# Performance work log

Measured on AMD Instinct MI355X. Metric: run time of the kernel, lower is better.

## Reference

```python
import jax, jax.numpy as jnp
import numpy as np

N, E, ESM, H, OUT, L, NG = 20000, 640000, 1280, 128, 256, 3, 64
NV, EV = 4, 1  # node/edge vector channels
MSG_S, MSG_V = 2 * H + H, 2 * NV + EV   # 384, 9
UPD_S, UPD_V = 2 * H, 2 * NV            # 256, 8


def _safe_norm(v):
    # exact ||v|| with zero (not nan) gradient at v == 0
    n2 = jnp.sum(v * v, axis=-1)
    pos = n2 > 0
    return jnp.sqrt(jnp.where(pos, n2, 1.0)) * pos


def _normalize(x, eps=1e-12):
    n = _safe_norm(x)[..., None]
    return jnp.where(n > 0, x / jnp.maximum(n, eps), 0.0)


def _ln(x, g, b, eps=1e-5):
    m = x.mean(-1, keepdims=True)
    v = ((x - m) ** 2).mean(-1, keepdims=True)
    return (x - m) / jnp.sqrt(v + eps) * g + b


def _gvp(s, v, Wss, Wvs, Wsv, Wvv, g, b):
    # s: [M, Cs], v: [M, Cv, 3]
    vn = _safe_norm(v)                                        # [M, Cv]
    s_out = jax.nn.gelu(_ln(s @ Wss.T + vn @ Wvs.T, g, b), approximate=False)
    v_out = jnp.einsum('mic,oi->moc', v, Wvv)                 # [M, Cvo, 3]
    v_out = v_out * jax.nn.sigmoid(s @ Wsv.T)[:, :, None]     # gate from input s
    return s_out, v_out


def _compute_node_vectors(coords, cb):
    ca_cb = _normalize(cb - coords)
    ca_next = jnp.roll(coords, -1, axis=0)
    d = (ca_next - coords).at[-1].set(0.0)
    d = _normalize(d)
    normal = _normalize(jnp.cross(ca_cb, d))
    t = (ca_next - jnp.roll(coords, 1, axis=0)).at[0].set(0.0).at[-1].set(0.0)
    t = _normalize(t)
    return jnp.stack([ca_cb, d, normal, t], axis=1)           # [N, 4, 3]


def setup_inputs() -> dict:
    key = jax.random.key(0)
    ks = jax.random.split(key, 32)

    def w(k, shape):
        return (jax.random.normal(k, shape, jnp.float32) / np.sqrt(shape[-1])).astype(jnp.float32)

    inp = {
        'esm_features': jax.random.normal(ks[0], (N, ESM), jnp.float32),
        'geometric_features': jax.random.normal(ks[1], (N, 15), jnp.float32),
        'node_coords': jax.random.normal(ks[2], (N, 3), jnp.float32) * 10.0,
        'edge_index': jax.random.randint(ks[3], (2, E), 0, N, jnp.int32),
        'edge_attr': jax.random.normal(ks[4], (E, 16), jnp.float32),
        'batch_index': jnp.sort(jax.random.randint(ks[5], (N,), 0, NG, jnp.int32)),
        # projections
        'node_proj_W': w(ks[6], (H, ESM + 9)), 'node_proj_b': jnp.zeros((H,), jnp.float32),
        'edge_proj_W': w(ks[7], (H, 13)), 'edge_proj_b': jnp.zeros((H,), jnp.float32),
        # message GVP (stacked over L layers)
        'msg_Wss': w(ks[8], (L, H, MSG_S)), 'msg_Wvs': w(ks[9], (L, H, MSG_V)),
        'msg_Wsv': w(ks[10], (L, NV, MSG_S)), 'msg_Wvv': w(ks[11], (L, NV, MSG_V)),
        'msg_ln_g': jnp.ones((L, H), jnp.float32), 'msg_ln_b': jnp.zeros((L, H), jnp.float32),
        # update GVP
        'upd_Wss': w(ks[12], (L, H, UPD_S)), 'upd_Wvs': w(ks[13], (L, H, UPD_V)),
        'upd_Wsv': w(ks[14], (L, NV, UPD_S)), 'upd_Wvv': w(ks[15], (L, NV, UPD_V)),
        'upd_ln_g': jnp.ones((L, H), jnp.float32), 'upd_ln_b': jnp.zeros((L, H), jnp.float32),
        # heads
        'node_out_W': w(ks[16], (ESM, H)), 'node_out_b': jnp.zeros((ESM,), jnp.float32),
        'graph_out_W': w(ks[17], (OUT, H)), 'graph_out_b': jnp.zeros((OUT,), jnp.float32),
    }
    return inp


def reference(esm_features, geometric_features, node_coords, edge_index, edge_attr,
              batch_index, node_proj_W, node_proj_b, edge_proj_W, edge_proj_b,
              msg_Wss, msg_Wvs, msg_Wsv, msg_Wvv, msg_ln_g, msg_ln_b,
              upd_Wss, upd_Wvs, upd_Wsv, upd_Wvv, upd_ln_g, upd_ln_b,
              node_out_W, node_out_b, graph_out_W, graph_out_b):
    n = esm_features.shape[0]
    cb = geometric_features[:, 3:6]
    geo_scalar = geometric_features[:, 6:15]
    node_s = jnp.concatenate([esm_features, geo_scalar], -1) @ node_proj_W.T + node_proj_b
    node_v = _compute_node_vectors(node_coords, cb)
    edge_s = jnp.concatenate([edge_attr[:, 0:2], edge_attr[:, 5:]], -1) @ edge_proj_W.T + edge_proj_b
    edge_v = edge_attr[:, 2:5][:, None, :]                    # [E, 1, 3]
    src, dst = edge_index[0], edge_index[1]
    for l in range(msg_Wss.shape[0]):
        ms = jnp.concatenate([node_s[src], node_s[dst], edge_s], -1)   # [E, 3H]
        mv = jnp.concatenate([node_v[src], node_v[dst], edge_v], 1)    # [E, 9, 3]
        ms, mv = _gvp(ms, mv, msg_Wss[l], msg_Wvs[l], msg_Wsv[l], msg_Wvv[l],
                      msg_ln_g[l], msg_ln_b[l])
        ag_s = jnp.zeros((n, ms.shape[1]), ms.dtype).at[dst].add(ms)
        ag_v = jnp.zeros((n, mv.shape[1], 3), mv.dtype).at[dst].add(mv)
        us = jnp.concatenate([node_s, ag_s], -1)
        uv = jnp.concatenate([node_v, ag_v], 1)
        ns, nv = _gvp(us, uv, upd_Wss[l], upd_Wvs[l], upd_Wsv[l], upd_Wvv[l],
                      upd_ln_g[l], upd_ln_b[l])
        node_s = node_s + ns
        node_v = node_v + nv
    updated_nodes = node_s @ node_out_W.T + node_out_b
    gfeat = node_s @ graph_out_W.T + graph_out_b
    cnt = jax.ops.segment_sum(jnp.ones((n,), gfeat.dtype), batch_index, NG)
    graph_emb = jax.ops.segment_sum(gfeat, batch_index, NG) / jnp.maximum(cnt, 1.0)[:, None]
    return graph_emb, updated_nodes
```

## Files before the change

### kernel.cpp

```cpp
#include <hip/hip_runtime.h>
#include <math.h>

#define DEVI __device__ __forceinline__

namespace {

constexpr int NN = 20000;
constexpr int NE = 640000;

typedef __attribute__((ext_vector_type(8))) short s8v;
typedef __attribute__((ext_vector_type(4))) float f4v;

DEVI float gelu_f(float x){ return 0.5f*x*(1.0f+erff(x*0.70710678118654752440f)); }
DEVI float gelu_t(float x){
  float u = x*x;
  float z = x*(1.59576912f + 0.07135481f*u);
  return x / (1.f + __expf(-z));
}
DEVI float sigm(float x){ return 1.0f/(1.0f+expf(-x)); }
DEVI float sigm_f(float x){ return 1.0f/(1.0f+__expf(-x)); }
DEVI unsigned bf_rne(float f){ unsigned u=__float_as_uint(f); return (u + 0x7fffu + ((u>>16)&1u)) >> 16; }

struct F3{ float x,y,z; };
DEVI F3 sub3(F3 a, F3 b){ return F3{a.x-b.x, a.y-b.y, a.z-b.z}; }
DEVI F3 cross3(F3 a, F3 b){ return F3{a.y*b.z-a.z*b.y, a.z*b.x-a.x*b.z, a.x*b.y-a.y*b.x}; }
DEVI F3 snorm3(F3 v){
  float n2 = v.x*v.x+v.y*v.y+v.z*v.z;
  if(n2 > 0.f){ float inv = 1.0f/sqrtf(n2); return F3{v.x*inv, v.y*inv, v.z*inv}; }
  return F3{0.f,0.f,0.f};
}

__global__ void k_prep(const float* __restrict__ npW, const float* __restrict__ noW,
                       const float* __restrict__ goW,
                       const float* __restrict__ mWss, const float* __restrict__ mWvs,
                       const float* __restrict__ uWss, const float* __restrict__ uWvs,
                       unsigned short* __restrict__ npW_bf, float* __restrict__ Wt_no,
                       float* __restrict__ Wt_go,
                       float* __restrict__ Wt_mss, float* __restrict__ Wt_mvs,
                       float* __restrict__ Wt_uss, float* __restrict__ Wt_uvs){
  int b = blockIdx.x, t = threadIdx.x;
  if(b >= 1563){
    int idx = (b-1563)*256 + t;
    if(idx < 128*1289) npW_bf[idx] = (unsigned short)bf_rne(npW[idx]);
    return;
  }
  const float* src; float* dst; int R,C,ld,base,elems;
  if(b<640){ src=noW; dst=Wt_no; R=1280;C=128;ld=128; base=0; elems=163840; }
  else if(b<768){ src=goW; dst=Wt_go; R=256;C=128;ld=128; base=640; elems=32768; }
  else {
    int bb=b-768; int l=bb/265; int r=bb-l*265;
    if(r<128){ src=mWss+(size_t)l*128*384; dst=Wt_mss+(size_t)l*256*128; R=128;C=256;ld=384; base=768+l*265; elems=32768; }
    else if(r<133){ src=mWvs+(size_t)l*128*9; dst=Wt_mvs+(size_t)l*9*128; R=128;C=9;ld=9; base=768+l*265+128; elems=1152; }
    else if(r<261){ src=uWss+(size_t)l*128*256; dst=Wt_uss+(size_t)l*256*128; R=128;C=256;ld=256; base=768+l*265+133; elems=32768; }
    else { src=uWvs+(size_t)l*128*8; dst=Wt_uvs+(size_t)l*8*128; R=128;C=8;ld=8; base=768+l*265+261; elems=1024; }
  }
  int idx=(b-base)*256+t;
  if(idx>=elems) return;
  int r=idx/C, c=idx%C;
  dst[c*R+r] = src[r*ld+c];
}

__global__ __launch_bounds__(256,2) void k_init(
    const float* __restrict__ esm, const float* __restrict__ geo,
    const unsigned short* __restrict__ npW_bf, const float* __restrict__ bias,
    float* __restrict__ node_s){
  __shared__ unsigned short A_lds[64][136];
  __shared__ unsigned short B_lds[128][136];
  int t = threadIdx.x;
  int n0 = blockIdx.x*64;
  int wv = t>>6, lane = t&63;
  int kpair = t&63;
  int rb = t>>6;
  f4v acc[8];
#pragma unroll
  for(int i=0;i<8;i++) acc[i] = (f4v){0.f,0.f,0.f,0.f};
  for(int k0=0; k0<1408; k0+=128){
#pragma unroll
    for(int i=0;i<16;i++){
      int r = rb + 4*i;
      int row = n0 + r;
      int kk = k0 + 2*kpair;
      float v0=0.f, v1=0.f;
      if(row < NN){
        if(kk < 1280)        v0 = esm[(size_t)row*1280+kk];
        else if(kk < 1289)   v0 = geo[row*15+6+(kk-1280)];
        if(kk+1 < 1280)      v1 = esm[(size_t)row*1280+kk+1];
        else if(kk+1 < 1289) v1 = geo[row*15+6+(kk+1-1280)];
      }
      *reinterpret_cast<unsigned*>(&A_lds[r][2*kpair]) = bf_rne(v0) | (bf_rne(v1)<<16);
    }
#pragma unroll
    for(int i=0;i<32;i++){
      int o = rb + 4*i;
      int kk = k0 + 2*kpair;
      unsigned w0 = (kk<1289)   ? (unsigned)npW_bf[(size_t)o*1289+kk]   : 0u;
      unsigned w1 = (kk+1<1289) ? (unsigned)npW_bf[(size_t)o*1289+kk+1] : 0u;
      *reinterpret_cast<unsigned*>(&B_lds[o][2*kpair]) = w0 | (w1<<16);
    }
    __syncthreads();
    int arow = wv*16 + (lane&15);
    int kb = (lane>>4)*8;
#pragma unroll
    for(int s=0;s<4;s++){
      s8v a = *reinterpret_cast<const s8v*>(&A_lds[arow][s*32+kb]);
#pragma unroll
      for(int nt=0;nt<8;nt++){
        s8v b = *reinterpret_cast<const s8v*>(&B_lds[nt*16+(lane&15)][s*32+kb]);
        acc[nt] = __builtin_amdgcn_mfma_f32_16x16x32_bf16(a, b, acc[nt], 0,0,0);
      }
    }
    __syncthreads();
  }
  int col = lane&15;
  int r4 = (lane>>4)*4;
#pragma unroll
  for(int nt=0;nt<8;nt++){
    int o = nt*16+col;
    float bsv = bias[o];
#pragma unroll
    for(int r=0;r<4;r++){
      int row = n0 + wv*16 + r4 + r;
      if(row<NN) node_s[(size_t)row*128+o] = acc[nt][r] + bsv;
    }
  }
}

__global__ void k_nodevec(const float* __restrict__ coords, const float* __restrict__ geo,
                          float* __restrict__ node_v,
                          int* __restrict__ counts, int* __restrict__ cntg){
  int n = blockIdx.x*256 + threadIdx.x;
  if(n<64) cntg[n]=0;
  if(n>=NN) return;
  counts[n]=0;
  F3 c  {coords[n*3], coords[n*3+1], coords[n*3+2]};
  F3 cb {geo[n*15+3], geo[n*15+4], geo[n*15+5]};
  F3 cacb = snorm3(sub3(cb, c));
  F3 d{0.f,0.f,0.f};
  if(n < NN-1){
    F3 nx {coords[(n+1)*3], coords[(n+1)*3+1], coords[(n+1)*3+2]};
    d = snorm3(sub3(nx, c));
  }
  F3 nor = snorm3(cross3(cacb, d));
  F3 tv{0.f,0.f,0.f};
  if(n>0 && n<NN-1){
    F3 nx {coords[(n+1)*3], coords[(n+1)*3+1], coords[(n+1)*3+2]};
    F3 pv {coords[(n-1)*3], coords[(n-1)*3+1], coords[(n-1)*3+2]};
    tv = snorm3(sub3(nx, pv));
  }
  float* p = node_v + n*12;
  p[0]=cacb.x; p[1]=cacb.y; p[2]=cacb.z;
  p[3]=d.x;    p[4]=d.y;    p[5]=d.z;
  p[6]=nor.x;  p[7]=nor.y;  p[8]=nor.z;
  p[9]=tv.x;   p[10]=tv.y;  p[11]=tv.z;
}

__global__ void k_hist(const int* __restrict__ eidx, const int* __restrict__ batch,
                       int* __restrict__ counts, int* __restrict__ cntg){
  int i = blockIdx.x*256+threadIdx.x;
  if(i<NE) atomicAdd(&counts[eidx[NE+i]], 1);
  if(i<NN) atomicAdd(&cntg[batch[i]], 1);
}
__global__ void k_scan1(const int* __restrict__ counts, int* __restrict__ bsums){
  __shared__ int red[256];
  int b=blockIdx.x, t=threadIdx.x;
  int base=b*512;
  int v=0;
  for(int i=t;i<512;i+=256){ int g=base+i; if(g<NN) v+=counts[g]; }
  red[t]=v; __syncthreads();
  for(int s=128;s;s>>=1){ if(t<s) red[t]+=red[t+s]; __syncthreads(); }
  if(t==0) bsums[b]=red[0];
}
__global__ void k_scan23(const int* __restrict__ counts, const int* __restrict__ bsums,
                         int* __restrict__ offs, int* __restrict__ cursor){
  __shared__ int c_l[512];
  int b=blockIdx.x, t=threadIdx.x, base=b*512;
  for(int i=t;i<512;i+=256){ int g=base+i; c_l[i] = (g<NN)? counts[g]:0; }
  __syncthreads();
  if(t==0){
    int run=0;
    for(int i=0;i<b;i++) run += bsums[i];
    for(int i=0;i<512;i++){
      int g=base+i;
      if(g<NN){ offs[g]=run; cursor[g]=run; }
      run += c_l[i];
    }
    if(b==39) offs[NN]=run;
  }
}
__global__ void k_fill(const int* __restrict__ eidx, int* __restrict__ cursor,
                       const float* __restrict__ eattr,
                       int* __restrict__ srcp, float* __restrict__ ea_s){
  int e = blockIdx.x*256+threadIdx.x;
  if(e>=NE) return;
  int d = eidx[NE+e];
  int s = eidx[e];
  int pos = atomicAdd(&cursor[d], 1);
  srcp[pos] = s;
  const float4* src4 = reinterpret_cast<const float4*>(eattr + (size_t)e*16);
  float4* dst4 = reinterpret_cast<float4*>(ea_s + (size_t)pos*16);
  dst4[0]=src4[0]; dst4[1]=src4[1]; dst4[2]=src4[2]; dst4[3]=src4[3];
}

__global__ __launch_bounds__(256,4) void k_pre(
                      const float* __restrict__ node_s, const float* __restrict__ node_v,
                      const float* __restrict__ Wt_ss, const float* __restrict__ Wt_vs,
                      const float* __restrict__ Wsv, const float* __restrict__ Wvv,
                      float* __restrict__ P_a, float* __restrict__ P_b,
                      float* __restrict__ G_a, float* __restrict__ G_b,
                      float* __restrict__ V_a, float* __restrict__ V_b){
  __shared__ float s_l[16][128];
  __shared__ float nv_l[16][4];
  __shared__ float uv[16][12];
  int t = threadIdx.x;
  int n0 = blockIdx.x*16;
  for(int idx=t; idx<2048; idx+=256){
    int n = idx>>7, k = idx&127;
    s_l[n][k] = node_s[(size_t)(n0+n)*128 + k];
  }
  if(t<192){ int n=t/12, k=t%12; uv[n][k] = node_v[(n0+n)*12+k]; }
  __syncthreads();
  if(t<64){
    int n=t>>2, j=t&3;
    float x=uv[n][j*3], y=uv[n][j*3+1], z=uv[n][j*3+2];
    float n2=x*x+y*y+z*z;
    nv_l[n][j] = n2>0.f ? sqrtf(n2) : 0.f;
  }
  if(t<192){
    int n=t/12, k=t%12, c=k/3, x=k-c*3;
    float va=0.f, vb=0.f;
#pragma unroll
    for(int j=0;j<4;j++){
      float vv = uv[n][j*3+x];
      va += Wvv[c*9+j]*vv;
      vb += Wvv[c*9+4+j]*vv;
    }
    V_a[(n0+n)*12+k]=va; V_b[(n0+n)*12+k]=vb;
  }
  if(t<128){
    int n=t>>3, c=(t>>1)&3, hh=t&1;
    const float* w = Wsv + c*384 + hh*128;
    float g=0.f;
    for(int k=0;k<128;k+=4){
      float4 s4 = *reinterpret_cast<const float4*>(&s_l[n][k]);
      g = fmaf(s4.x,w[k],g); g = fmaf(s4.y,w[k+1],g);
      g = fmaf(s4.z,w[k+2],g); g = fmaf(s4.w,w[k+3],g);
    }
    (hh ? G_b : G_a)[(n0+n)*4+c] = g;
  }
  __syncthreads();
  int o = t&127, h = t>>7;
  float acc[16];
#pragma unroll
  for(int i=0;i<16;i++) acc[i]=0.f;
  const float* Wb = Wt_ss + h*128*128;
  for(int k=0;k<128;k+=4){
    float w0=Wb[(k+0)*128+o], w1=Wb[(k+1)*128+o], w2=Wb[(k+2)*128+o], w3=Wb[(k+3)*128+o];
#pragma unroll
    for(int n=0;n<16;n++){
      float4 s4 = *reinterpret_cast<const float4*>(&s_l[n][k]);
      acc[n] = fmaf(s4.x,w0,acc[n]); acc[n] = fmaf(s4.y,w1,acc[n]);
      acc[n] = fmaf(s4.z,w2,acc[n]); acc[n] = fmaf(s4.w,w3,acc[n]);
    }
  }
  const float* Wv = Wt_vs + h*4*128;
#pragma unroll
  for(int j=0;j<4;j++){
    float w = Wv[j*128+o];
#pragma unroll
    for(int n=0;n<16;n++) acc[n] += nv_l[n][j]*w;
  }
  float* P = h ? P_b : P_a;
#pragma unroll
  for(int n=0;n<16;n++) P[(size_t)(n0+n)*128+o] = acc[n];
}

__global__ void k_econst3(const float* __restrict__ mWss, const float* __restrict__ mWvs,
                          const float* __restrict__ mWsv, const float* __restrict__ mWvv,
                          const float* __restrict__ Wep, const float* __restrict__ epb,
                          float* __restrict__ econ){
  int l = blockIdx.x;
  const float* Wss = mWss + (size_t)l*128*384;
  const float* Wvs = mWvs + (size_t)l*128*9;
  const float* Wsv = mWsv + (size_t)l*4*384;
  const float* Wvv = mWvv + (size_t)l*4*9;
  float* ec = econ + (size_t)l*2048;
  int t=threadIdx.x;
  for(int idx=t; idx<13*128; idx+=256){
    int j=idx>>7, o=idx&127;
    float s=0.f;
    for(int k=0;k<128;k++) s += Wss[o*384+256+k]*Wep[k*13+j];
    ec[j*128+o]=s;
  }
  for(int o=t;o<128;o+=256){
    float s=0.f;
    for(int k=0;k<128;k++) s += Wss[o*384+256+k]*epb[k];
    ec[1664+o]=s;
    ec[1792+o]=Wvs[o*9+8];
  }
  if(t<52){ int c=t/13,j=t%13; float s=0.f; for(int k=0;k<128;k++) s+=Wsv[c*384+256+k]*Wep[k*13+j]; ec[1920+t]=s; }
  if(t<4){ float s=0.f; for(int k=0;k<128;k++) s+=Wsv[t*384+256+k]*epb[k]; ec[1972+t]=s; ec[1976+t]=Wvv[t*9+8]; }
}

__global__ __launch_bounds__(256,4) void k_edge(
    const float* __restrict__ ea_s, const float* __restrict__ ec,
    unsigned* __restrict__ preS2, float* __restrict__ preG){
  int t = threadIdx.x;
  int lane = t&63;
  int wid = blockIdx.x*4 + (t>>6);
  float mex[13], mey[13];
#pragma unroll
  for(int j=0;j<13;j++){ mex[j]=ec[j*128+lane]; mey[j]=ec[j*128+64+lane]; }
  float bx=ec[1664+lane], by=ec[1664+64+lane];
  float w8x=ec[1792+lane], w8y=ec[1792+64+lane];
  int cg = (lane<4)?lane:0;
  float grc[13];
#pragma unroll
  for(int j=0;j<13;j++) grc[j]=ec[1920+cg*13+j];
  float gb = ec[1972+cg];
  int e00 = wid*8;
#pragma unroll 2
  for(int i=0;i<8;i++){
    int e = e00+i;
    const float4* ea = reinterpret_cast<const float4*>(ea_s + (size_t)e*16);
    float4 A0=ea[0], A1=ea[1], A2=ea[2], A3=ea[3];
    float e0=A0.x,e1=A0.y,e2=A1.y,e3=A1.z,e4=A1.w,
          e5=A2.x,e6=A2.y,e7=A2.z,e8=A2.w,e9=A3.x,
          e10=A3.y,e11=A3.z,e12=A3.w;
    float evx=A0.z, evy=A0.w, evz=A1.x;
    float en2 = evx*evx+evy*evy+evz*evz;
    float evn = en2>0.f ? sqrtf(en2) : 0.f;
    float px = fmaf(evn,w8x,bx);
    float py = fmaf(evn,w8y,by);
    px=fmaf(mex[0],e0,px);   py=fmaf(mey[0],e0,py);
    px=fmaf(mex[1],e1,px);   py=fmaf(mey[1],e1,py);
    px=fmaf(mex[2],e2,px);   py=fmaf(mey[2],e2,py);
    px=fmaf(mex[3],e3,px);   py=fmaf(mey[3],e3,py);
    px=fmaf(mex[4],e4,px);   py=fmaf(mey[4],e4,py);
    px=fmaf(mex[5],e5,px);   py=fmaf(mey[5],e5,py);
    px=fmaf(mex[6],e6,px);   py=fmaf(mey[6],e6,py);
    px=fmaf(mex[7],e7,px);   py=fmaf(mey[7],e7,py);
    px=fmaf(mex[8],e8,px);   py=fmaf(mey[8],e8,py);
    px=fmaf(mex[9],e9,px);   py=fmaf(mey[9],e9,py);
    px=fmaf(mex[10],e10,px); py=fmaf(mey[10],e10,py);
    px=fmaf(mex[11],e11,px); py=fmaf(mey[11],e11,py);
    px=fmaf(mex[12],e12,px); py=fmaf(mey[12],e12,py);
    preS2[(size_t)e*64+lane] = bf_rne(px) | (bf_rne(py)<<16);
    if(lane<4){
      float g=gb;
      g=fmaf(grc[0],e0,g);  g=fmaf(grc[1],e1,g);  g=fmaf(grc[2],e2,g);
      g=fmaf(grc[3],e3,g);  g=fmaf(grc[4],e4,g);  g=fmaf(grc[5],e5,g);
      g=fmaf(grc[6],e6,g);  g=fmaf(grc[7],e7,g);  g=fmaf(grc[8],e8,g);
      g=fmaf(grc[9],e9,g);  g=fmaf(grc[10],e10,g); g=fmaf(grc[11],e11,g);
      g=fmaf(grc[12],e12,g);
      preG[(size_t)e*8+lane] = g;
    } else if(lane<7){
      float evv = (lane==4)?evx:((lane==5)?evy:evz);
      preG[(size_t)e*8+lane] = evv;
    }
  }
}

#define DECLST(P) unsigned P##w=0; float P##pax=0.f,P##pay=0.f,P##g8=0.f,P##ev=0.f,P##ga=0.f,P##va=0.f;
#define LOADST(P, IDX) do{ int _p=(IDX); int _s=srcp[_p]; \
  P##w   = preS2[(size_t)_p*64 + lane]; \
  P##pax = P_a[(size_t)_s*128+lane]; P##pay = P_a[(size_t)_s*128+64+lane]; \
  if(lane<12){ P##g8 = preG[(size_t)_p*8+cv]; P##ev = preG[(size_t)_p*8+4+xv]; \
               P##ga = G_a[(size_t)_s*4+cv];  P##va = V_a[(size_t)_s*12+lane]; } \
}while(0)
#define COMPUTE(P) do{ \
  float px = __uint_as_float(P##w<<16); \
  float py = __uint_as_float(P##w & 0xffff0000u); \
  float pre0 = px + P##pax + PBx; \
  float pre1 = py + P##pay + PBy; \
  float sm = pre0+pre1; \
  float sq = pre0*pre0 + pre1*pre1; \
  _Pragma("unroll") \
  for(int m=32;m;m>>=1){ sm += __shfl_xor(sm,m); sq += __shfl_xor(sq,m); } \
  float mean = sm*0.0078125f; \
  float var  = fmaf(sq,0.0078125f, -mean*mean); \
  float rstd = rsqrtf((var>0.f?var:0.f) + 1e-5f); \
  accx += gelu_t(fmaf((pre0-mean)*rstd, LGx, LBx)); \
  accy += gelu_t(fmaf((pre1-mean)*rstd, LGy, LBy)); \
  if(lane<12){ \
    float g = P##g8 + P##ga + gbn; \
    float gt = sigm_f(g); \
    avk = fmaf(fmaf(wvc, P##ev, P##va + vbk), gt, avk); \
  } \
}while(0)

__global__ __launch_bounds__(256,4) void k_msg(
                      const float* __restrict__ P_a, const float* __restrict__ P_b,
                      const float* __restrict__ G_a, const float* __restrict__ G_b,
                      const float* __restrict__ V_a, const float* __restrict__ V_b,
                      const unsigned* __restrict__ preS2, const float* __restrict__ preG,
                      const int* __restrict__ srcp, const int* __restrict__ offs,
                      const float* __restrict__ ec,
                      const float* __restrict__ lng, const float* __restrict__ lnb,
                      float* __restrict__ ag_s, float* __restrict__ ag_v){
  int t = threadIdx.x;
  int n = blockIdx.x*4 + (t>>6);
  int lane = t&63;
  float PBx = P_b[(size_t)n*128+lane], PBy = P_b[(size_t)n*128+64+lane];
  float LGx = lng[lane], LGy = lng[64+lane];
  float LBx = lnb[lane], LBy = lnb[64+lane];
  int cv = lane/3, xv = lane - cv*3;
  float vbk=0.f, gbn=0.f, wvc=0.f;
  if(lane<12){
    vbk = V_b[(size_t)n*12+lane];
    gbn = G_b[(size_t)n*4+cv];
    wvc = ec[1976+cv];
  }
  float accx=0.f, accy=0.f, avk=0.f;
  int beg = offs[n], end = offs[n+1];
  DECLST(a_) DECLST(b_)
  int idx = beg;
  if(beg < end) LOADST(a_, beg);
  while(idx + 1 < end){
    LOADST(b_, idx+1);
    COMPUTE(a_);
    if(idx + 2 < end) LOADST(a_, idx+2);
    COMPUTE(b_);
    idx += 2;
  }
  if(idx < end) COMPUTE(a_);
  ag_s[(size_t)n*128+lane]    = accx;
  ag_s[(size_t)n*128+64+lane] = accy;
  if(lane<12) ag_v[(size_t)n*12+lane] = avk;
}

__global__ __launch_bounds__(256,4) void k_update(
                         float* __restrict__ node_s, float* __restrict__ node_v,
                         const float* __restrict__ ag_s, const float* __restrict__ ag_v,
                         const float* __restrict__ Wt_ss, const float* __restrict__ Wt_vs,
                         const float* __restrict__ Wsv, const float* __restrict__ Wvv,
                         const float* __restrict__ lng, const float* __restrict__ lnb){
  __shared__ float us[16][260];
  __shared__ float pre[16][129];
  __shared__ float uv[16][24];
  __shared__ float uvn[16][8];
  __shared__ float stats[16][2];
  __shared__ float gate_l[16][4];
  int t = threadIdx.x;
  int n0 = blockIdx.x*16;
  for(int idx=t; idx<2048; idx+=256){
    int n = idx>>7, k = idx&127;
    us[n][k]     = node_s[(size_t)(n0+n)*128+k];
    us[n][128+k] = ag_s[(size_t)(n0+n)*128+k];
  }
  for(int idx=t; idx<384; idx+=256){
    int n = idx/24, k = idx%24;
    uv[n][k] = (k<12) ? node_v[(n0+n)*12+k] : ag_v[(n0+n)*12 + (k-12)];
  }
  __syncthreads();
  if(t<128){
    int n=t>>3, j=t&7;
    float x=uv[n][j*3], y=uv[n][j*3+1], z=uv[n][j*3+2];
    float n2=x*x+y*y+z*z;
    uvn[n][j] = n2>0.f ? sqrtf(n2) : 0.f;
  }
  __syncthreads();
  int o = t&127, h = t>>7;
  float acc[8];
#pragma unroll
  for(int i=0;i<8;i++) acc[i]=0.f;
  for(int k=0;k<256;k+=4){
    float w0=Wt_ss[(k+0)*128+o], w1=Wt_ss[(k+1)*128+o], w2=Wt_ss[(k+2)*128+o], w3=Wt_ss[(k+3)*128+o];
#pragma unroll
    for(int i=0;i<8;i++){
      float4 s4 = *reinterpret_cast<const float4*>(&us[h*8+i][k]);
      acc[i] = fmaf(s4.x,w0,acc[i]); acc[i] = fmaf(s4.y,w1,acc[i]);
      acc[i] = fmaf(s4.z,w2,acc[i]); acc[i] = fmaf(s4.w,w3,acc[i]);
    }
  }
#pragma unroll
  for(int j=0;j<8;j++){
    float w = Wt_vs[j*128+o];
#pragma unroll
    for(int i=0;i<8;i++) acc[i] += uvn[h*8+i][j]*w;
  }
#pragma unroll
  for(int i=0;i<8;i++) pre[h*8+i][o] = acc[i];
  __syncthreads();
  {
    int n = t>>4, p = t&15;
    float s=0.f;
#pragma unroll
    for(int q=0;q<8;q++) s += pre[n][p*8+q];
#pragma unroll
    for(int m=8;m;m>>=1) s += __shfl_xor(s,m);
    float mean = s*(1.f/128.f);
    float v=0.f;
#pragma unroll
    for(int q=0;q<8;q++){ float d=pre[n][p*8+q]-mean; v += d*d; }
#pragma unroll
    for(int m=8;m;m>>=1) v += __shfl_xor(v,m);
    if(p==0){ stats[n][0]=mean; stats[n][1]=rsqrtf(v*(1.f/128.f)+1e-5f); }
  }
  __syncthreads();
  {
    float LG = lng[o], LB = lnb[o];
#pragma unroll
    for(int i=0;i<8;i++){
      int n = h*8+i;
      float hh = (pre[n][o]-stats[n][0])*stats[n][1]*LG + LB;
      node_s[(size_t)(n0+n)*128+o] += gelu_f(hh);
    }
  }
  {
    int n = t>>4, c = t&3, p = (t>>2)&3;
    float g=0.f;
    int kb = p*64;
    for(int k=0;k<64;k+=4){
      float4 s4 = *reinterpret_cast<const float4*>(&us[n][kb+k]);
      g = fmaf(s4.x,Wsv[c*256+kb+k],g);   g = fmaf(s4.y,Wsv[c*256+kb+k+1],g);
      g = fmaf(s4.z,Wsv[c*256+kb+k+2],g); g = fmaf(s4.w,Wsv[c*256+kb+k+3],g);
    }
    g += __shfl_xor(g,4);
    g += __shfl_xor(g,8);
    if(p==0) gate_l[n][c] = sigm(g);
  }
  __syncthreads();
  if(t<192){
    int n = t/12, k = t%12, c = k/3, x = k-c*3;
    float s=0.f;
#pragma unroll
    for(int j=0;j<8;j++) s += Wvv[c*8+j]*uv[n][j*3+x];
    node_v[(n0+n)*12+k] += s*gate_l[n][c];
  }
}

__global__ __launch_bounds__(256,4) void k_outg(
                      const float* __restrict__ node_s, const float* __restrict__ Wt_no,
                      const float* __restrict__ nob, const float* __restrict__ Wt_go,
                      const int* __restrict__ batch, float* __restrict__ gacc,
                      float* __restrict__ out){
  __shared__ float s_l[16][128];
  __shared__ int b_l[16];
  int t = threadIdx.x;
  int n0 = blockIdx.x*16;
  int y = blockIdx.y;
  for(int idx=t; idx<2048; idx+=256){
    int n=idx>>7, k=idx&127;
    s_l[n][k] = node_s[(size_t)(n0+n)*128+k];
  }
  if(y==5 && t<16) b_l[t]=batch[n0+t];
  __syncthreads();
  if(y<5){
    int o = y*256 + t;
    float acc[16];
#pragma unroll
    for(int i=0;i<16;i++) acc[i]=0.f;
    for(int k=0;k<128;k+=4){
      float w0=Wt_no[(k+0)*1280+o], w1=Wt_no[(k+1)*1280+o], w2=Wt_no[(k+2)*1280+o], w3=Wt_no[(k+3)*1280+o];
#pragma unroll
      for(int n=0;n<16;n++){
        float4 s4 = *reinterpret_cast<const float4*>(&s_l[n][k]);
        acc[n] = fmaf(s4.x,w0,acc[n]); acc[n] = fmaf(s4.y,w1,acc[n]);
        acc[n] = fmaf(s4.z,w2,acc[n]); acc[n] = fmaf(s4.w,w3,acc[n]);
      }
    }
    float b = nob[o];
#pragma unroll
    for(int n=0;n<16;n++) out[16384 + (size_t)(n0+n)*1280 + o] = acc[n]+b;
  } else {
    int o=t;
    float acc[16];
#pragma unroll
    for(int i=0;i<16;i++) acc[i]=0.f;
    for(int k=0;k<128;k+=4){
      float w0=Wt_go[(k+0)*256+o], w1=Wt_go[(k+1)*256+o], w2=Wt_go[(k+2)*256+o], w3=Wt_go[(k+3)*256+o];
#pragma unroll
      for(int n=0;n<16;n++){
        float4 s4 = *reinterpret_cast<const float4*>(&s_l[n][k]);
        acc[n] = fmaf(s4.x,w0,acc[n]); acc[n] = fmaf(s4.y,w1,acc[n]);
        acc[n] = fmaf(s4.z,w2,acc[n]); acc[n] = fmaf(s4.w,w3,acc[n]);
      }
    }
    float run=0.f; int cur=b_l[0];
#pragma unroll
    for(int n=0;n<16;n++){
      int g=b_l[n];
      if(g!=cur){ atomicAdd(&gacc[cur*256+o], run); run=0.f; cur=g; }
      run += acc[n];
    }
    atomicAdd(&gacc[cur*256+o], run);
  }
}

__global__ void k_gfin(const float* __restrict__ gacc, const int* __restrict__ cntg,
                       const float* __restrict__ gob, float* __restrict__ out){
  int g=blockIdx.x, o=threadIdx.x;
  int c=cntg[g];
  out[g*256+o] = (c>0) ? (gacc[g*256+o]/(float)c + gob[o]) : 0.f;
}

}

extern "C" void kernel_launch(void* const* d_in, const int* in_sizes, int n_in,
                              void* d_out, int out_size, void* d_ws, size_t ws_size,
                              hipStream_t stream){
  (void)in_sizes; (void)n_in; (void)out_size;
  const float* esm   = (const float*)d_in[0];
  const float* geo   = (const float*)d_in[1];
  const float* coords= (const float*)d_in[2];
  const int*   eidx  = (const int*)d_in[3];
  const float* eattr = (const float*)d_in[4];
  const int*   batch = (const int*)d_in[5];
  const float* npW   = (const float*)d_in[6];
  const float* npb   = (const float*)d_in[7];
  const float* epW   = (const float*)d_in[8];
  const float* epb   = (const float*)d_in[9];
  const float* mWss  = (const float*)d_in[10];
  const float* mWvs  = (const float*)d_in[11];
  const float* mWsv  = (const float*)d_in[12];
  const float* mWvv  = (const float*)d_in[13];
  const float* mlg   = (const float*)d_in[14];
  const float* mlb   = (const float*)d_in[15];
  const float* uWss  = (const float*)d_in[16];
  const float* uWvs  = (const float*)d_in[17];
  const float* uWsv  = (const float*)d_in[18];
  const float* uWvv  = (const float*)d_in[19];
  const float* ulg   = (const float*)d_in[20];
  const float* ulb   = (const float*)d_in[21];
  const float* noW   = (const float*)d_in[22];
  const float* nob   = (const float*)d_in[23];
  const float* goW   = (const float*)d_in[24];
  const float* gob   = (const float*)d_in[25];
  float* out = (float*)d_out;

  char* base = (char*)d_ws;
  size_t off = 0;
  auto ALLOC = [&](size_t bytes)->char*{
    char* p = base + off;
    off = (off + bytes + 255) & ~(size_t)255;
    return p;
  };
  float* node_s = (float*)ALLOC((size_t)NN*128*4);
  float* P_a    = (float*)ALLOC((size_t)NN*128*4);
  float* P_b    = (float*)ALLOC((size_t)NN*128*4);
  float* ag_s   = (float*)ALLOC((size_t)NN*128*4);
  float* node_v = (float*)ALLOC((size_t)NN*12*4);
  float* ag_v   = (float*)ALLOC((size_t)NN*12*4);
  float* V_a    = (float*)ALLOC((size_t)NN*12*4);
  float* V_b    = (float*)ALLOC((size_t)NN*12*4);
  float* G_a    = (float*)ALLOC((size_t)NN*4*4);
  float* G_b    = (float*)ALLOC((size_t)NN*4*4);
  unsigned short* npW_bf = (unsigned short*)ALLOC((size_t)128*1289*2);
  float* Wt_no  = (float*)ALLOC((size_t)128*1280*4);
  float* Wt_go  = (float*)ALLOC((size_t)128*256*4);
  float* Wt_mss = (float*)ALLOC((size_t)3*256*128*4);
  float* Wt_mvs = (float*)ALLOC((size_t)3*9*128*4);
  float* Wt_uss = (float*)ALLOC((size_t)3*256*128*4);
  float* Wt_uvs = (float*)ALLOC((size_t)3*8*128*4);
  float* econ   = (float*)ALLOC((size_t)3*2048*4);
  float* gacc   = (float*)ALLOC((size_t)64*256*4);
  int* counts = (int*)ALLOC((size_t)NN*4);
  int* offs   = (int*)ALLOC((size_t)(NN+1)*4);
  int* cursor = (int*)ALLOC((size_t)NN*4);
  int* bsums  = (int*)ALLOC((size_t)64*4);
  int* cntg   = (int*)ALLOC((size_t)64*4);
  int* srcp   = (int*)ALLOC((size_t)NE*4);
  float* ea_s = (float*)ALLOC((size_t)NE*16*4);
  unsigned* preS2 = (unsigned*)ALLOC((size_t)NE*64*4);
  float* preG     = (float*)ALLOC((size_t)NE*8*4);
  if(off > ws_size) return;

  hipMemsetAsync(gacc, 0, (size_t)64*256*4, stream);

  k_prep<<<2208,256,0,stream>>>(npW, noW, goW, mWss, mWvs, uWss, uWvs,
                                npW_bf, Wt_no, Wt_go, Wt_mss, Wt_mvs, Wt_uss, Wt_uvs);
  k_init<<<313,256,0,stream>>>(esm, geo, npW_bf, npb, node_s);
  k_nodevec<<<79,256,0,stream>>>(coords, geo, node_v, counts, cntg);
  k_hist<<<2500,256,0,stream>>>(eidx, batch, counts, cntg);
  k_scan1<<<40,256,0,stream>>>(counts, bsums);
  k_scan23<<<40,256,0,stream>>>(counts, bsums, offs, cursor);
  k_fill<<<2500,256,0,stream>>>(eidx, cursor, eattr, srcp, ea_s);
  k_econst3<<<3,256,0,stream>>>(mWss, mWvs, mWsv, mWvv, epW, epb, econ);

  for(int l=0;l<3;l++){
    k_pre<<<1250,256,0,stream>>>(node_s, node_v,
                                 Wt_mss + (size_t)l*256*128, Wt_mvs + (size_t)l*9*128,
                                 mWsv + (size_t)l*4*384, mWvv + (size_t)l*4*9,
                                 P_a, P_b, G_a, G_b, V_a, V_b);
    k_edge<<<20000,256,0,stream>>>(ea_s, econ + (size_t)l*2048, preS2, preG);
    k_msg<<<5000,256,0,stream>>>(P_a, P_b, G_a, G_b, V_a, V_b, preS2, preG, srcp, offs,
                                 econ + (size_t)l*2048, mlg + (size_t)l*128, mlb + (size_t)l*128,
                                 ag_s, ag_v);
    k_update<<<1250,256,0,stream>>>(node_s, node_v, ag_s, ag_v,
                                    Wt_uss + (size_t)l*256*128, Wt_uvs + (size_t)l*8*128,
                                    uWsv + (size_t)l*4*256, uWvv + (size_t)l*4*8,
                                    ulg + (size_t)l*128, ulb + (size_t)l*128);
  }
  k_outg<<<dim3(1250,6),256,0,stream>>>(node_s, Wt_no, nob, Wt_go, batch, gacc, out);
  k_gfin<<<64,256,0,stream>>>(gacc, cntg, gob, out);
}
```

Measured before the change: 1.705 ms.

## Pre-convert ESM to bf16 and split-K the input projection GEMM

Adds a separate conversion kernel that writes the ESM and geometric features as a padded bf16 matrix, and pads the projection weights to the same K. The input projection GEMM now reads operands straight from global memory with vectorized loads, without LDS staging or barriers, and splits K four ways to raise the block count. A new reduce kernel sums the four partials, adds the bias, and writes node_s, reusing the preS2 buffer as scratch. This is meant to remove the serialized, poorly coalesced load-and-convert path in the old GEMM, at the cost of an extra bf16 copy of the inputs and partial-sum traffic through memory.

Result: faster. 1.627 ms (-4.6%).

```diff
diff --git a/kernel.cpp b/kernel.cpp
--- a/kernel.cpp
+++ b/kernel.cpp
@@ -41,7 +41,10 @@
   int b = blockIdx.x, t = threadIdx.x;
   if(b >= 1563){
     int idx = (b-1563)*256 + t;
-    if(idx < 128*1289) npW_bf[idx] = (unsigned short)bf_rne(npW[idx]);
+    if(idx < 128*1408){
+      int r = idx/1408, c = idx-r*1408;
+      npW_bf[idx] = (c<1289) ? (unsigned short)bf_rne(npW[(size_t)r*1289+c]) : (unsigned short)0;
+    }
     return;
   }
   const float* src; float* dst; int R,C,ld,base,elems;
@@ -60,69 +63,77 @@
   dst[c*R+r] = src[r*ld+c];
 }
 
-__global__ __launch_bounds__(256,2) void k_init(
-    const float* __restrict__ esm, const float* __restrict__ geo,
-    const unsigned short* __restrict__ npW_bf, const float* __restrict__ bias,
-    float* __restrict__ node_s){
-  __shared__ unsigned short A_lds[64][136];
-  __shared__ unsigned short B_lds[128][136];
+__global__ void k_conv(const float* __restrict__ esm, const float* __restrict__ geo,
+                       unsigned short* __restrict__ esm_bf){
+  int idx = blockIdx.x*256 + threadIdx.x;
+  if(idx >= 20000*176) return;
+  int r = idx/176, c = idx - r*176;
+  int k = c*8;
+  float v0,v1,v2,v3,v4,v5,v6,v7;
+  if(k+8 <= 1280){
+    const float4* p = reinterpret_cast<const float4*>(esm + (size_t)r*1280 + k);
+    float4 x=p[0], y=p[1];
+    v0=x.x;v1=x.y;v2=x.z;v3=x.w;v4=y.x;v5=y.y;v6=y.z;v7=y.w;
+  } else {
+    float vv[8];
+#pragma unroll
+    for(int j=0;j<8;j++){
+      int kk=k+j;
+      vv[j] = (kk<1280)? esm[(size_t)r*1280+kk] : ((kk<1289)? geo[r*15+6+(kk-1280)] : 0.f);
+    }
+    v0=vv[0];v1=vv[1];v2=vv[2];v3=vv[3];v4=vv[4];v5=vv[5];v6=vv[6];v7=vv[7];
+  }
+  uint4 w;
+  w.x = bf_rne(v0) | (bf_rne(v1)<<16);
+  w.y = bf_rne(v2) | (bf_rne(v3)<<16);
+  w.z = bf_rne(v4) | (bf_rne(v5)<<16);
+  w.w = bf_rne(v6) | (bf_rne(v7)<<16);
+  reinterpret_cast<uint4*>(esm_bf)[idx] = w;
+}
+
+__global__ __launch_bounds__(256,4) void k_init(
+    const unsigned short* __restrict__ esm_bf, const unsigned short* __restrict__ npW_bf,
+    float* __restrict__ part){
   int t = threadIdx.x;
-  int n0 = blockIdx.x*64;
+  int b = blockIdx.x;
+  int ks = b & 3, nb = b >> 2;
   int wv = t>>6, lane = t&63;
-  int kpair = t&63;
-  int rb = t>>6;
+  int row0 = nb*64 + wv*16;
+  int arow = row0 + (lane&15);
+  int arc = (arow < NN) ? arow : (NN-1);
+  int kb = (lane>>4)*8;
+  const unsigned short* ap = esm_bf + (size_t)arc*1408 + ks*352 + kb;
+  const unsigned short* bp = npW_bf + (size_t)(lane&15)*1408 + ks*352 + kb;
   f4v acc[8];
 #pragma unroll
   for(int i=0;i<8;i++) acc[i] = (f4v){0.f,0.f,0.f,0.f};
-  for(int k0=0; k0<1408; k0+=128){
-#pragma unroll
-    for(int i=0;i<16;i++){
-      int r = rb + 4*i;
-      int row = n0 + r;
-      int kk = k0 + 2*kpair;
-      float v0=0.f, v1=0.f;
-      if(row < NN){
-        if(kk < 1280)        v0 = esm[(size_t)row*1280+kk];
-        else if(kk < 1289)   v0 = geo[row*15+6+(kk-1280)];
-        if(kk+1 < 1280)      v1 = esm[(size_t)row*1280+kk+1];
-        else if(kk+1 < 1289) v1 = geo[row*15+6+(kk+1-1280)];
-      }
-      *reinterpret_cast<unsigned*>(&A_lds[r][2*kpair]) = bf_rne(v0) | (bf_rne(v1)<<16);
-    }
-#pragma unroll
-    for(int i=0;i<32;i++){
-      int o = rb + 4*i;
-      int kk = k0 + 2*kpair;
-      unsigned w0 = (kk<1289)   ? (unsigned)npW_bf[(size_t)o*1289+kk]   : 0u;
-      unsigned w1 = (kk+1<1289) ? (unsigned)npW_bf[(size_t)o*1289+kk+1] : 0u;
-      *reinterpret_cast<unsigned*>(&B_lds[o][2*kpair]) = w0 | (w1<<16);
-    }
-    __syncthreads();
-    int arow = wv*16 + (lane&15);
-    int kb = (lane>>4)*8;
-#pragma unroll
-    for(int s=0;s<4;s++){
-      s8v a = *reinterpret_cast<const s8v*>(&A_lds[arow][s*32+kb]);
-#pragma unroll
-      for(int nt=0;nt<8;nt++){
-        s8v b = *reinterpret_cast<const s8v*>(&B_lds[nt*16+(lane&15)][s*32+kb]);
-        acc[nt] = __builtin_amdgcn_mfma_f32_16x16x32_bf16(a, b, acc[nt], 0,0,0);
-      }
-    }
-    __syncthreads();
-  }
-  int col = lane&15;
-  int r4 = (lane>>4)*4;
+  for(int c=0;c<11;c++){
+    s8v a = *reinterpret_cast<const s8v*>(ap + c*32);
+#pragma unroll
+    for(int nt=0;nt<8;nt++){
+      s8v bb = *reinterpret_cast<const s8v*>(bp + (size_t)nt*16*1408 + c*32);
+      acc[nt] = __builtin_amdgcn_mfma_f32_16x16x32_bf16(a, bb, acc[nt], 0,0,0);
+    }
+  }
+  float* po = part + (size_t)ks*NN*128;
+  int col = lane&15, r4 = (lane>>4)*4;
 #pragma unroll
   for(int nt=0;nt<8;nt++){
     int o = nt*16+col;
-    float bsv = bias[o];
 #pragma unroll
     for(int r=0;r<4;r++){
-      int row = n0 + wv*16 + r4 + r;
-      if(row<NN) node_s[(size_t)row*128+o] = acc[nt][r] + bsv;
-    }
-  }
+      int row = row0 + r4 + r;
+      if(row<NN) po[(size_t)row*128+o] = acc[nt][r];
+    }
+  }
+}
+
+__global__ void k_reduce(const float* __restrict__ part, const float* __restrict__ bias,
+                         float* __restrict__ node_s){
+  int idx = blockIdx.x*256 + threadIdx.x;
+  int o = idx & 127;
+  node_s[idx] = bias[o] + part[idx] + part[(size_t)NN*128+idx]
+              + part[2*(size_t)NN*128+idx] + part[3*(size_t)NN*128+idx];
 }
 
 __global__ void k_nodevec(const float* __restrict__ coords, const float* __restrict__ geo,
@@ -645,7 +656,8 @@
   float* V_b    = (float*)ALLOC((size_t)NN*12*4);
   float* G_a    = (float*)ALLOC((size_t)NN*4*4);
   float* G_b    = (float*)ALLOC((size_t)NN*4*4);
-  unsigned short* npW_bf = (unsigned short*)ALLOC((size_t)128*1289*2);
+  unsigned short* npW_bf = (unsigned short*)ALLOC((size_t)128*1408*2);
+  unsigned short* esm_bf = (unsigned short*)ALLOC((size_t)NN*1408*2);
   float* Wt_no  = (float*)ALLOC((size_t)128*1280*4);
   float* Wt_go  = (float*)ALLOC((size_t)128*256*4);
   float* Wt_mss = (float*)ALLOC((size_t)3*256*128*4);
@@ -664,12 +676,15 @@
   unsigned* preS2 = (unsigned*)ALLOC((size_t)NE*64*4);
   float* preG     = (float*)ALLOC((size_t)NE*8*4);
   if(off > ws_size) return;
+  float* part = (float*)preS2;
 
   hipMemsetAsync(gacc, 0, (size_t)64*256*4, stream);
 
-  k_prep<<<2208,256,0,stream>>>(npW, noW, goW, mWss, mWvs, uWss, uWvs,
+  k_prep<<<2267,256,0,stream>>>(npW, noW, goW, mWss, mWvs, uWss, uWvs,
                                 npW_bf, Wt_no, Wt_go, Wt_mss, Wt_mvs, Wt_uss, Wt_uvs);
-  k_init<<<313,256,0,stream>>>(esm, geo, npW_bf, npb, node_s);
+  k_conv<<<13750,256,0,stream>>>(esm, geo, esm_bf);
+  k_init<<<1252,256,0,stream>>>(esm_bf, npW_bf, part);
+  k_reduce<<<10000,256,0,stream>>>(part, npb, node_s);
   k_nodevec<<<79,256,0,stream>>>(coords, geo, node_v, counts, cntg);
   k_hist<<<2500,256,0,stream>>>(eidx, batch, counts, cntg);
   k_scan1<<<40,256,0,stream>>>(counts, bsums);
```
